# Performance work log

Measured on AMD Instinct MI355X. Metric: run time of the kernel, lower is better.

The kernel has to match this reference:

```python
import jax, jax.numpy as jnp
import numpy as np

B, T, L, H = 8, 32, 512, 768  # batch docs, decode steps, encoder length, BART-base hidden


def setup_inputs() -> dict:
    key = jax.random.key(0)
    ks = jax.random.split(key, 7)
    sc = 1.0 / np.sqrt(H).astype(np.float32)
    return {
        "encoder_hn": jax.random.normal(ks[0], (B, L, H), jnp.float32),
        "dec": jax.random.normal(ks[1], (B, T, H), jnp.float32),   # decoder_rnn outputs per step
        "W1": jax.random.normal(ks[2], (H, H), jnp.float32) * sc,  # nnW1 (no bias)
        "W2": jax.random.normal(ks[3], (H, H), jnp.float32) * sc,  # nnW2 (no bias)
        "v": jax.random.normal(ks[4], (H,), jnp.float32) * sc,     # nnV (no bias)
        "starts": jax.random.randint(ks[5], (B, T), 0, 128, jnp.int32),  # ragged slice start per step
        "lens": jax.random.randint(ks[6], (B,), 300, L + 1, jnp.int32),  # curL per document
    }


def reference(encoder_hn, dec, W1, W2, v, starts, lens):
    # pointerLayer batched over (b, t):
    #   WE = nnW1(en)          -> [B, L, H]
    #   WD = nnW2(di expanded) -> [B, T, H]
    #   scores = selu( nnV( selu(WE + WD) ) )  over positions [start, len)
    WE = jnp.einsum('blh,kh->blk', encoder_hn, W1)                 # [B, L, H]
    WD = jnp.einsum('bth,kh->btk', dec, W2)                        # [B, T, H]
    act = jax.nn.selu(WE[:, None, :, :] + WD[:, :, None, :])      # [B, T, L, H]
    scores = jax.nn.selu(jnp.einsum('btlh,h->btl', act, v))       # [B, T, L]
    # ragged slice curencoder_hn[start:curL] expressed as a mask
    pos = jnp.arange(L, dtype=jnp.int32)
    mask = (pos[None, None, :] >= starts[:, :, None]) & \
           (pos[None, None, :] < lens[:, None, None])              # [B, T, L]
    NEG = jnp.asarray(-1e30, scores.dtype)
    logp = jax.nn.log_softmax(jnp.where(mask, scores, NEG), axis=-1)
    return jnp.where(mask, logp, jnp.zeros((), logp.dtype))       # masked log-probs [B, T, L]
```

## Files before the change

### kernel.cpp

```cpp
#include <hip/hip_runtime.h>
#include <math.h>

constexpr int Bn = 8, Tn = 32, Ln = 512, Hn = 768;

typedef __attribute__((ext_vector_type(8))) short bf16x8;
typedef __attribute__((ext_vector_type(4))) float f32x4;

__device__ __forceinline__ short f2bf(float x) {
    unsigned u = __float_as_uint(x);
    u += 0x7FFFu + ((u >> 16) & 1u);
    return (short)(u >> 16);
}
__device__ __forceinline__ float bf2f(unsigned short s) {
    return __uint_as_float(((unsigned)s) << 16);
}

constexpr float kScale = 1.0507009873554804934193349852946f;
constexpr float kAS    = 1.7580993408473768f;

__device__ __forceinline__ float selu(float x) {
    return x > 0.f ? kScale * x : fmaf(kAS, __expf(x), -kAS);
}

__global__ __launch_bounds__(256) void cvt_bf16_multi(
    const float* __restrict__ s0, short* __restrict__ d0, int c0,
    const float* __restrict__ s1, short* __restrict__ d1, int c1,
    const float* __restrict__ s2, short* __restrict__ d2, int c2,
    const float* __restrict__ s3, short* __restrict__ d3, int c3)
{
    const int i = blockIdx.x * 256 + threadIdx.x;
    if (i >= c3) return;
    const float* s; short* d; int off;
    if (i < c0)      { s = s0; d = d0; off = i; }
    else if (i < c1) { s = s1; d = d1; off = i - c0; }
    else if (i < c2) { s = s2; d = d2; off = i - c1; }
    else             { s = s3; d = d3; off = i - c2; }
    const float4 f = ((const float4*)s)[off];
    short4 r;
    r.x = f2bf(f.x); r.y = f2bf(f.y); r.z = f2bf(f.z); r.w = f2bf(f.w);
    ((short4*)d)[off] = r;
}

__global__ __launch_bounds__(256) void gemm2_bf16_nt(
    const short* __restrict__ A1, const short* __restrict__ B1,
    unsigned short* __restrict__ C1, int M1,
    const short* __restrict__ A2, const short* __restrict__ B2,
    unsigned short* __restrict__ C2,
    int N, int K)
{
    constexpr int BM = 128, BN = 128, BK = 32;
    __shared__ __align__(16) short As[BM * BK];
    __shared__ __align__(16) short Bs[BN * BK];

    const int nblk1 = M1 / BM;
    const int bx = blockIdx.x;
    const short* A; const short* Bm; unsigned short* C; int bm;
    if (bx < nblk1) { A = A1; Bm = B1; C = C1; bm = bx * BM; }
    else            { A = A2; Bm = B2; C = C2; bm = (bx - nblk1) * BM; }
    const int bn = blockIdx.y * BN;

    const int tid  = threadIdx.x;
    const int lane = tid & 63;
    const int wv   = tid >> 6;
    const int quad = lane >> 4;
    const int l16  = lane & 15;
    const int wm   = (wv & 1) * 64;
    const int wn   = (wv >> 1) * 64;

    const int sr = lane >> 2;
    const int kq = (lane & 3) << 3;

    f32x4 acc[4][4] = {};

    for (int k0 = 0; k0 < K; k0 += BK) {
        const int ra = wv * 16 + sr;
        __builtin_amdgcn_global_load_lds(
            (const __attribute__((address_space(1))) unsigned int*)(A + (size_t)(bm + ra) * K + k0 + kq),
            (__attribute__((address_space(3))) unsigned int*)(As + ra * BK + kq), 16, 0, 0);
        __builtin_amdgcn_global_load_lds(
            (const __attribute__((address_space(1))) unsigned int*)(A + (size_t)(bm + 64 + ra) * K + k0 + kq),
            (__attribute__((address_space(3))) unsigned int*)(As + (64 + ra) * BK + kq), 16, 0, 0);
        __builtin_amdgcn_global_load_lds(
            (const __attribute__((address_space(1))) unsigned int*)(Bm + (size_t)(bn + ra) * K + k0 + kq),
            (__attribute__((address_space(3))) unsigned int*)(Bs + ra * BK + kq), 16, 0, 0);
        __builtin_amdgcn_global_load_lds(
            (const __attribute__((address_space(1))) unsigned int*)(Bm + (size_t)(bn + 64 + ra) * K + k0 + kq),
            (__attribute__((address_space(3))) unsigned int*)(Bs + (64 + ra) * BK + kq), 16, 0, 0);
        __syncthreads();

        bf16x8 af[4], bfr[4];
#pragma unroll
        for (int i = 0; i < 4; ++i)
            af[i] = *(const bf16x8*)&As[(wm + i * 16 + l16) * BK + quad * 8];
#pragma unroll
        for (int j = 0; j < 4; ++j)
            bfr[j] = *(const bf16x8*)&Bs[(wn + j * 16 + l16) * BK + quad * 8];
#pragma unroll
        for (int i = 0; i < 4; ++i)
#pragma unroll
            for (int j = 0; j < 4; ++j)
                acc[i][j] = __builtin_amdgcn_mfma_f32_16x16x32_bf16(af[i], bfr[j], acc[i][j], 0, 0, 0);
        __syncthreads();
    }

#pragma unroll
    for (int i = 0; i < 4; ++i)
#pragma unroll
        for (int j = 0; j < 4; ++j)
#pragma unroll
            for (int rr = 0; rr < 4; ++rr) {
                const int row = bm + wm + i * 16 + quad * 4 + rr;
                const int col = bn + wn + j * 16 + l16;
                C[(size_t)row * N + col] = (unsigned short)f2bf(acc[i][j][rr]);
            }
}

__global__ __launch_bounds__(256) void scores_kernel(
    const unsigned short* __restrict__ WE,
    const unsigned short* __restrict__ WD,
    const float* __restrict__ v,
    float* __restrict__ sc)
{
    const int bid = blockIdx.x;
    const int b = bid & 7;
    const int r = bid >> 3;
    const int t = r & 31;
    const int chunk = r >> 5;
    const int bt = b * Tn + t;
    const int lane = threadIdx.x & 63;
    const int wv = threadIdx.x >> 6;
    const int l0 = chunk * 64 + wv * 16;

    float wdr[12], vr[12];
#pragma unroll
    for (int j = 0; j < 3; ++j) {
        const int h = (lane << 2) + (j << 8);
        const ushort4 wdu = *(const ushort4*)(WD + (size_t)bt * Hn + h);
        const float4 vv = *(const float4*)(v + h);
        wdr[j * 4 + 0] = bf2f(wdu.x); wdr[j * 4 + 1] = bf2f(wdu.y);
        wdr[j * 4 + 2] = bf2f(wdu.z); wdr[j * 4 + 3] = bf2f(wdu.w);
        vr[j * 4 + 0] = vv.x; vr[j * 4 + 1] = vv.y;
        vr[j * 4 + 2] = vv.z; vr[j * 4 + 3] = vv.w;
    }

    const unsigned short* WEb = WE + (size_t)b * Ln * Hn;

#pragma unroll
    for (int g = 0; g < 4; ++g) {
        const int lg = l0 + g * 4;
        ushort4 weu[4][3];
#pragma unroll
        for (int rr = 0; rr < 4; ++rr) {
            const unsigned short* row = WEb + (size_t)(lg + rr) * Hn;
#pragma unroll
            for (int j = 0; j < 3; ++j)
                weu[rr][j] = *(const ushort4*)(row + (lane << 2) + (j << 8));
        }
        float s[4] = {0.f, 0.f, 0.f, 0.f};
#pragma unroll
        for (int j = 0; j < 3; ++j) {
#pragma unroll
            for (int rr = 0; rr < 4; ++rr) {
                float x;
                x = bf2f(weu[rr][j].x) + wdr[j * 4 + 0]; s[rr] = fmaf(selu(x), vr[j * 4 + 0], s[rr]);
                x = bf2f(weu[rr][j].y) + wdr[j * 4 + 1]; s[rr] = fmaf(selu(x), vr[j * 4 + 1], s[rr]);
                x = bf2f(weu[rr][j].z) + wdr[j * 4 + 2]; s[rr] = fmaf(selu(x), vr[j * 4 + 2], s[rr]);
                x = bf2f(weu[rr][j].w) + wdr[j * 4 + 3]; s[rr] = fmaf(selu(x), vr[j * 4 + 3], s[rr]);
            }
        }
#pragma unroll
        for (int off = 32; off > 0; off >>= 1) {
#pragma unroll
            for (int rr = 0; rr < 4; ++rr)
                s[rr] += __shfl_xor(s[rr], off, 64);
        }
        if (lane == 0) {
#pragma unroll
            for (int rr = 0; rr < 4; ++rr)
                sc[(size_t)bt * Ln + lg + rr] = selu(s[rr]);
        }
    }
}

__global__ __launch_bounds__(512) void softmax_kernel(
    const float* __restrict__ sc,
    const int* __restrict__ starts,
    const int* __restrict__ lens,
    float* __restrict__ out)
{
    __shared__ float red[16];
    const int bt = blockIdx.x;
    const int b = bt / Tn;
    const int tid = threadIdx.x;
    const int lane = tid & 63;
    const int wv = tid >> 6;

    const int start = starts[bt];
    const int len = lens[b];
    const int l = tid;
    const bool msk = (l >= start) && (l < len);
    const float val = sc[(size_t)bt * Ln + l];

    float mx = msk ? val : -1e30f;
#pragma unroll
    for (int off = 32; off > 0; off >>= 1)
        mx = fmaxf(mx, __shfl_xor(mx, off, 64));
    if (lane == 0) red[wv] = mx;
    __syncthreads();
    mx = red[0];
#pragma unroll
    for (int i = 1; i < 8; ++i) mx = fmaxf(mx, red[i]);

    float sm = msk ? __expf(val - mx) : 0.f;
#pragma unroll
    for (int off = 32; off > 0; off >>= 1)
        sm += __shfl_xor(sm, off, 64);
    if (lane == 0) red[8 + wv] = sm;
    __syncthreads();
    float tot = red[8];
#pragma unroll
    for (int i = 1; i < 8; ++i) tot += red[8 + i];

    const float logZ = mx + __logf(tot);
    out[(size_t)bt * Ln + l] = msk ? (val - logZ) : 0.f;
}

extern "C" void kernel_launch(void* const* d_in, const int* in_sizes, int n_in,
                              void* d_out, int out_size, void* d_ws, size_t ws_size,
                              hipStream_t stream) {
    const float* enc    = (const float*)d_in[0];
    const float* dec    = (const float*)d_in[1];
    const float* W1     = (const float*)d_in[2];
    const float* W2     = (const float*)d_in[3];
    const float* v      = (const float*)d_in[4];
    const int*   starts = (const int*)d_in[5];
    const int*   lens   = (const int*)d_in[6];
    float* out = (float*)d_out;

    constexpr int n_enc = Bn * Ln * Hn;
    constexpr int n_dec = Bn * Tn * Hn;
    constexpr int n_w   = Hn * Hn;
    constexpr int n_sc  = Bn * Tn * Ln;

    const size_t need = (size_t)(n_enc + n_dec + 2 * n_w) * 2
                      + (size_t)(n_enc + n_dec) * 2
                      + (size_t)n_sc * 4;
    if (ws_size < need) return;

    short* enc16 = (short*)d_ws;
    short* dec16 = enc16 + n_enc;
    short* w1_16 = dec16 + n_dec;
    short* w2_16 = w1_16 + n_w;
    unsigned short* WE16 = (unsigned short*)(w2_16 + n_w);
    unsigned short* WD16 = WE16 + n_enc;
    float* sc = (float*)(WD16 + n_dec);

    constexpr int c0 = n_enc / 4;
    constexpr int c1 = c0 + n_dec / 4;
    constexpr int c2 = c1 + n_w / 4;
    constexpr int c3 = c2 + n_w / 4;
    cvt_bf16_multi<<<dim3((c3 + 255) / 256), dim3(256), 0, stream>>>(
        enc, enc16, c0, dec, dec16, c1, W1, w1_16, c2, W2, w2_16, c3);

    gemm2_bf16_nt<<<dim3((Bn * Ln) / 128 + (Bn * Tn) / 128, Hn / 128),
                    dim3(256), 0, stream>>>(
        enc16, w1_16, WE16, Bn * Ln,
        dec16, w2_16, WD16, Hn, Hn);

    scores_kernel<<<dim3(2048), dim3(256), 0, stream>>>(WE16, WD16, v, sc);
    softmax_kernel<<<dim3(Bn * Tn), dim3(512), 0, stream>>>(sc, starts, lens, out);
}
```

Before: 130.4 us.

## Fuse scores and softmax into one per-(b,t) block, skipping masked rows

Merges the scores kernel and the softmax kernel into a single 512-thread block per (b,t). Scores are kept in shared memory instead of a global scratch buffer, and groups of positions that lie entirely outside [start, len) are skipped, so their WE rows are never read. The grid shrinks from 2048 blocks to 256, which may lower parallelism and occupancy on a large GPU. Each block now walks all 512 positions serially across its 8 waves.

```diff
diff --git a/kernel.cpp b/kernel.cpp
--- a/kernel.cpp
+++ b/kernel.cpp
@@ -115,21 +115,27 @@
             }
 }
 
-__global__ __launch_bounds__(256) void scores_kernel(
+__global__ __launch_bounds__(512) void scores_softmax_fused(
     const unsigned short* __restrict__ WE,
     const unsigned short* __restrict__ WD,
     const float* __restrict__ v,
-    float* __restrict__ sc)
+    const int* __restrict__ starts,
+    const int* __restrict__ lens,
+    float* __restrict__ out)
 {
     const int bid = blockIdx.x;
     const int b = bid & 7;
-    const int r = bid >> 3;
-    const int t = r & 31;
-    const int chunk = r >> 5;
+    const int t = bid >> 3;
     const int bt = b * Tn + t;
-    const int lane = threadIdx.x & 63;
-    const int wv = threadIdx.x >> 6;
-    const int l0 = chunk * 64 + wv * 16;
+    const int tid = threadIdx.x;
+    const int lane = tid & 63;
+    const int wv = tid >> 6;
+
+    __shared__ float sc[Ln];
+    __shared__ float red[16];
+
+    const int start = starts[bt];
+    const int len = lens[b];
 
     float wdr[12], vr[12];
 #pragma unroll
@@ -145,9 +151,11 @@
 
     const unsigned short* WEb = WE + (size_t)b * Ln * Hn;
 
-#pragma unroll
-    for (int g = 0; g < 4; ++g) {
-        const int lg = l0 + g * 4;
+    for (int k = 0; k < 16; ++k) {
+        const int g = wv + (k << 3);
+        const int lg = g << 2;
+        if (lg + 3 < start || lg >= len) continue;
+
         ushort4 weu[4][3];
 #pragma unroll
         for (int rr = 0; rr < 4; ++rr) {
@@ -177,31 +185,16 @@
         if (lane == 0) {
 #pragma unroll
             for (int rr = 0; rr < 4; ++rr)
-                sc[(size_t)bt * Ln + lg + rr] = selu(s[rr]);
+                sc[lg + rr] = selu(s[rr]);
         }
     }
-}
-
-__global__ __launch_bounds__(512) void softmax_kernel(
-    const float* __restrict__ sc,
-    const int* __restrict__ starts,
-    const int* __restrict__ lens,
-    float* __restrict__ out)
-{
-    __shared__ float red[16];
-    const int bt = blockIdx.x;
-    const int b = bt / Tn;
-    const int tid = threadIdx.x;
-    const int lane = tid & 63;
-    const int wv = tid >> 6;
-
-    const int start = starts[bt];
-    const int len = lens[b];
+    __syncthreads();
+
     const int l = tid;
     const bool msk = (l >= start) && (l < len);
-    const float val = sc[(size_t)bt * Ln + l];
-
-    float mx = msk ? val : -1e30f;
+    const float val = msk ? sc[l] : -1e30f;
+
+    float mx = val;
 #pragma unroll
     for (int off = 32; off > 0; off >>= 1)
         mx = fmaxf(mx, __shfl_xor(mx, off, 64));
@@ -240,11 +233,9 @@
     constexpr int n_enc = Bn * Ln * Hn;
     constexpr int n_dec = Bn * Tn * Hn;
     constexpr int n_w   = Hn * Hn;
-    constexpr int n_sc  = Bn * Tn * Ln;
 
     const size_t need = (size_t)(n_enc + n_dec + 2 * n_w) * 2
-                      + (size_t)(n_enc + n_dec) * 2
-                      + (size_t)n_sc * 4;
+                      + (size_t)(n_enc + n_dec) * 2;
     if (ws_size < need) return;
 
     short* enc16 = (short*)d_ws;
@@ -253,7 +244,6 @@
     short* w2_16 = w1_16 + n_w;
     unsigned short* WE16 = (unsigned short*)(w2_16 + n_w);
     unsigned short* WD16 = WE16 + n_enc;
-    float* sc = (float*)(WD16 + n_dec);
 
     constexpr int c0 = n_enc / 4;
     constexpr int c1 = c0 + n_dec / 4;
@@ -267,6 +257,6 @@
         enc16, w1_16, WE16, Bn * Ln,
         dec16, w2_16, WD16, Hn, Hn);
 
-    scores_kernel<<<dim3(2048), dim3(256), 0, stream>>>(WE16, WD16, v, sc);
-    softmax_kernel<<<dim3(Bn * Tn), dim3(512), 0, stream>>>(sc, starts, lens, out);
-}
+    scores_softmax_fused<<<dim3(Bn * Tn), dim3(512), 0, stream>>>(
+        WE16, WD16, v, starts, lens, out);
+}
```

Result: no change. 129.2 us (-0.8%).
